# Kernel optimization log

Hardware: AMD Instinct MI355X
Metric: run time of the kernel (lower is better)

Reference implementation:

```python
import jax, jax.numpy as jnp
import numpy as np

F_SIZE = 8          # filter_size (even, >4 -> sinc mode)
C, H, W = 3, 720, 1280


def setup_inputs() -> dict:
    key = jax.random.key(0)
    k1, k2 = jax.random.split(key)
    x = jax.random.normal(k1, (1, C, H, W), dtype=jnp.float32)
    # optical flow in absolute pixels; a few pixels of motion is realistic
    flow = jax.random.normal(k2, (1, 2, H, W), dtype=jnp.float32) * 4.0
    return {"x": x, "flow": flow}


def _sinc_coeffs(s, offsets):
    # s: [H, W] fractional displacement in [0, 1); offsets: [F]
    # window * sinc interpolation coefficients -> [F, H, W]
    t = s[None, :, :] - offsets[:, None, None]
    return jnp.cos(jnp.pi * t / F_SIZE) * jnp.sinc(t)


def reference(x, flow):
    # Warper.forward in training mode (module default): q_flow = flow (no
    # fractional_accuracy rounding, which only applies in eval mode).
    _, C_, H_, W_ = x.shape
    fs = F_SIZE
    # neighbor tap offsets: -fs//2+1 .. fs//2  (e.g. -3..4 for fs=8)
    offsets = jnp.arange(-(fs // 2) + 1, fs // 2 + 1, dtype=jnp.float32)

    fx = flow[0, 0]  # horizontal (column) flow [H, W]
    fy = flow[0, 1]  # vertical (row) flow    [H, W]
    rfx = jnp.floor(fx)
    rfy = jnp.floor(fy)
    sx = fx - rfx    # fractional part in [0, 1)
    sy = fy - rfy

    col = jnp.arange(W_, dtype=jnp.float32)[None, :]   # [1, W]
    row = jnp.arange(H_, dtype=jnp.float32)[:, None]   # [H, 1]
    # integer neighbor coordinates, clamped (padding_mode='border') [F, H, W]
    ix = jnp.clip(col[None] + rfx[None] + offsets[:, None, None], 0, W_ - 1).astype(jnp.int32)
    iy = jnp.clip(row[None] + rfy[None] + offsets[:, None, None], 0, H_ - 1).astype(jnp.int32)

    x0 = x[0]  # [C, H, W]
    # multi-tap gather: [C, F_i, F_j, H, W] (nearest grid_sample of integer coords)
    gathered = x0[:, iy[:, None, :, :], ix[None, :, :, :]]

    cx = _sinc_coeffs(sx, offsets)  # [F, H, W] horizontal coefficients
    cy = _sinc_coeffs(sy, offsets)  # [F, H, W] vertical coefficients
    # separable interpolation: sum over j (columns) then i (rows), fused
    out = jnp.einsum('cijhw,jhw,ihw->chw', gathered, cx, cy)
    return out[None]  # [1, C, H, W]
```

## Files before the change

### kernel.cpp

```cpp
#include <hip/hip_runtime.h>
#include <math.h>

#define CC 3
#define HH 720
#define WW 1280
#define HW (HH * WW)

#define TW 64
#define TH 16
#define GX (WW / TW)
#define GY (HH / TH)
#define NWG (GX * GY)

#define SW 1288
#define PLANE (HH * SW)
#define WS_HALFS (6 * PLANE + 8)
#define WS_BYTES ((size_t)WS_HALFS * 2)

#define RMAX 16
#define NKEY 97

typedef float f4 __attribute__((ext_vector_type(4), aligned(4)));
typedef _Float16 h8 __attribute__((ext_vector_type(8), aligned(4)));
typedef _Float16 h2v __attribute__((ext_vector_type(2)));

#if __has_builtin(__builtin_amdgcn_fdot2)
#define HAVE_FDOT2 1
#endif

__constant__ float COSK[8] = {0.38268343f, 0.70710678f, 0.92387953f, 1.0f,
                              0.92387953f, 0.70710678f, 0.38268343f, 0.0f};
__constant__ float SINK[8] = {-0.92387953f, -0.70710678f, -0.38268343f, 0.0f,
                              0.38268343f, 0.70710678f, 0.92387953f, 1.0f};
__constant__ float SGNK[8] = {-1.0f, 1.0f, -1.0f, 1.0f, -1.0f, 1.0f, -1.0f, 1.0f};

__device__ __forceinline__ void sinc_weights(float s, float* wgt) {
    const float PI = 3.14159265358979f;
    float sp = __sinf(PI * s);
    float s8, c8;
    __sincosf(PI * s * 0.125f, &s8, &c8);
#pragma unroll
    for (int j = 0; j < 8; ++j) {
        float t = s - (float)(j - 3);
        float win = c8 * COSK[j] + s8 * SINK[j];
        float r = (t == 0.0f) ? 1.0f : __fdividef(sp * SGNK[j], PI * t);
        wgt[j] = win * r;
    }
}

__device__ __forceinline__ float dot8f(h8 v, const h2v* cw) {
#ifdef HAVE_FDOT2
    h2v* p = (h2v*)&v;
    float a = __builtin_amdgcn_fdot2(p[0], cw[0], 0.0f, false);
    a = __builtin_amdgcn_fdot2(p[1], cw[1], a, false);
    a = __builtin_amdgcn_fdot2(p[2], cw[2], a, false);
    a = __builtin_amdgcn_fdot2(p[3], cw[3], a, false);
    return a;
#else
    float r = 0.f;
#pragma unroll
    for (int j = 0; j < 8; ++j)
        r = fmaf((float)v[j], (float)cw[j >> 1][j & 1], r);
    return r;
#endif
}

__global__ __launch_bounds__(256) void conv_kernel(const float* __restrict__ x,
                                                   _Float16* __restrict__ ws) {
    int tid = blockIdx.x * blockDim.x + threadIdx.x;
    if (tid >= CC * HH * (WW / 4)) return;
    int k4 = tid % (WW / 4);
    int rest = tid / (WW / 4);
    int k = k4 * 4;
    f4 v = *(const f4*)(x + rest * WW + k);
    int dst = rest * SW + k;
    _Float16 a = (_Float16)v.x, b = (_Float16)v.y,
             c = (_Float16)v.z, d = (_Float16)v.w;
    typedef _Float16 h4 __attribute__((ext_vector_type(4), aligned(8)));
    *(h4*)(ws + dst) = (h4){a, b, c, d};
    _Float16* wb = ws + 3 * PLANE + 1 + dst;
    wb[0] = a; wb[1] = b; wb[2] = c; wb[3] = d;
}

__device__ __forceinline__ void pixel_slow(const float* __restrict__ x,
                                           int bx, int by,
                                           const float* cxw, const float* cyw,
                                           float& r0, float& r1, float& r2) {
    int xcl[8];
#pragma unroll
    for (int j = 0; j < 8; ++j) xcl[j] = min(max(bx + (j - 3), 0), WW - 1);
    r0 = 0.f; r1 = 0.f; r2 = 0.f;
#pragma unroll
    for (int i = 0; i < 8; ++i) {
        int o = min(max(by + (i - 3), 0), HH - 1) * WW;
        float cyi = cyw[i];
        const float* p0 = x + o;
        const float* p1 = p0 + HW;
        const float* p2 = p1 + HW;
        float rs0 = 0.f, rs1 = 0.f, rs2 = 0.f;
#pragma unroll
        for (int j = 0; j < 8; ++j) {
            float cj = cxw[j];
            rs0 = fmaf(p0[xcl[j]], cj, rs0);
            rs1 = fmaf(p1[xcl[j]], cj, rs1);
            rs2 = fmaf(p2[xcl[j]], cj, rs2);
        }
        r0 = fmaf(cyi, rs0, r0);
        r1 = fmaf(cyi, rs1, r1);
        r2 = fmaf(cyi, rs2, r2);
    }
}

__global__ __launch_bounds__(1024) void warp_kernel(const float* __restrict__ x,
                                                    const float* __restrict__ flow,
                                                    const _Float16* __restrict__ hx,
                                                    float* __restrict__ out) {
    __shared__ float sfx[1024], sfy[1024];
    __shared__ unsigned short sid[1024];
    __shared__ int HIST[128], SC[128], CUR[128];

    int tid = threadIdx.x;

    int bid = blockIdx.x;
    const int q = NWG / 8, r = NWG % 8;
    int xcd = bid & 7;
    int swz = (xcd < r ? xcd * (q + 1) : r * (q + 1) + (xcd - r) * q) + (bid >> 3);
    int tx = swz % GX;
    int ty = swz / GX;
    int w0 = tx * TW;
    int h0 = ty * TH;

    if (tid < 128) HIST[tid] = 0;
    __syncthreads();

    int w = w0 + (tid & 63);
    int h = h0 + (tid >> 6);
    int idx = h * WW + w;
    float fx = flow[idx];
    float fy = flow[HW + idx];
    sfx[tid] = fx;
    sfy[tid] = fy;
    {
        float rfx = floorf(fx), rfy = floorf(fy);
        int ix = (int)rfx, iy = (int)rfy;
        int s = w + ix - 3;
        int by = h + iy;
        bool fast = (iy >= -RMAX) && (iy <= RMAX) && (s >= 0) && (s <= WW - 8);
        int key = fast ? ((by - (h0 - RMAX)) * 2 + (s & 1)) : (NKEY - 1);
        atomicAdd(&HIST[key], 1);
    }
    __syncthreads();

    if (tid < 128) SC[tid] = HIST[tid];
    __syncthreads();
    for (int d = 1; d < 128; d <<= 1) {
        int v = 0;
        if (tid < 128 && tid >= d) v = SC[tid - d];
        __syncthreads();
        if (tid < 128) SC[tid] += v;
        __syncthreads();
    }
    if (tid < 128) CUR[tid] = SC[tid] - HIST[tid];
    __syncthreads();

    {
        float rfx = floorf(fx), rfy = floorf(fy);
        int ix = (int)rfx, iy = (int)rfy;
        int s = w + ix - 3;
        int by = h + iy;
        bool fast = (iy >= -RMAX) && (iy <= RMAX) && (s >= 0) && (s <= WW - 8);
        int key = fast ? ((by - (h0 - RMAX)) * 2 + (s & 1)) : (NKEY - 1);
        int pos = atomicAdd(&CUR[key], 1);
        sid[pos] = (unsigned short)tid;
    }
    __syncthreads();

    int me = sid[tid];
    float mfx = sfx[me], mfy = sfy[me];
    int mw = w0 + (me & 63);
    int mh = h0 + (me >> 6);
    float rfx = floorf(mfx), rfy = floorf(mfy);
    float sx = mfx - rfx, sy = mfy - rfy;
    int ix = (int)rfx, iy = (int)rfy;
    int s = mw + ix - 3;
    int by = mh + iy;
    bool fast = (iy >= -RMAX) && (iy <= RMAX) && (s >= 0) && (s <= WW - 8);

    float cxw[8], cyw[8];
    sinc_weights(sx, cxw);
    sinc_weights(sy, cyw);

    float r0, r1, r2;
    if (fast) {
        h2v cwp[4];
#pragma unroll
        for (int j = 0; j < 4; ++j)
            cwp[j] = (h2v){(_Float16)cxw[2 * j], (_Float16)cxw[2 * j + 1]};
        const _Float16* hp = hx + ((s & 1) ? (3 * PLANE + 1) : 0) + s;
        int ro[8];
#pragma unroll
        for (int i = 0; i < 8; ++i)
            ro[i] = min(max(by + (i - 3), 0), HH - 1) * SW;
        r0 = r1 = r2 = 0.f;
#pragma unroll
        for (int i = 0; i < 8; ++i) {
            h8 v0 = *(const h8*)(hp + ro[i]);
            h8 v1 = *(const h8*)(hp + ro[i] + PLANE);
            h8 v2 = *(const h8*)(hp + ro[i] + 2 * PLANE);
            float cyi = cyw[i];
            r0 = fmaf(cyi, dot8f(v0, cwp), r0);
            r1 = fmaf(cyi, dot8f(v1, cwp), r1);
            r2 = fmaf(cyi, dot8f(v2, cwp), r2);
        }
    } else {
        pixel_slow(x, mw + ix, mh + iy, cxw, cyw, r0, r1, r2);
    }

    int oidx = mh * WW + mw;
    out[oidx] = r0;
    out[HW + oidx] = r1;
    out[2 * HW + oidx] = r2;
}

__global__ __launch_bounds__(256) void warp_kernel_f32(const float* __restrict__ x,
                                                       const float* __restrict__ flow,
                                                       float* __restrict__ out) {
    int idx = blockIdx.x * blockDim.x + threadIdx.x;
    if (idx >= HW) return;
    int w = idx % WW;
    int h = idx / WW;
    float fx = flow[idx], fy = flow[HW + idx];
    float rfx = floorf(fx), rfy = floorf(fy);
    int bx = w + (int)rfx, by = h + (int)rfy;
    float cxw[8], cyw[8];
    sinc_weights(fx - rfx, cxw);
    sinc_weights(fy - rfy, cyw);
    float r0, r1, r2;
    pixel_slow(x, bx, by, cxw, cyw, r0, r1, r2);
    out[idx] = r0;
    out[HW + idx] = r1;
    out[2 * HW + idx] = r2;
}

extern "C" void kernel_launch(void* const* d_in, const int* in_sizes, int n_in,
                              void* d_out, int out_size, void* d_ws, size_t ws_size,
                              hipStream_t stream) {
    const float* x = (const float*)d_in[0];
    const float* flow = (const float*)d_in[1];
    float* out = (float*)d_out;

    if (ws_size >= WS_BYTES) {
        _Float16* ws = (_Float16*)d_ws;
        int nconv = CC * HH * (WW / 4);
        conv_kernel<<<(nconv + 255) / 256, 256, 0, stream>>>(x, ws);
        warp_kernel<<<NWG, 1024, 0, stream>>>(x, flow, ws, out);
    } else {
        warp_kernel_f32<<<(HW + 255) / 256, 256, 0, stream>>>(x, flow, out);
    }
}
```

Baseline: 53.93 us.

## Shrink warp tiles, use wave-shuffle scan, and software-pipeline fp16 channel loads

Halves the tile height so each block has 512 threads, and sizes the histogram keys to match. The multi-barrier LDS prefix scan becomes a single-wave shuffle scan, and the XCD swizzle is simplified because NWG is now divisible by 8. In the fast path, all row loads for one channel are issued before the sinc weights are computed, and each channel's loads overlap the previous channel's dot products. This hides gather latency and cuts barrier overhead, at the cost of more live registers for the v/u buffers.

```diff
diff --git a/kernel.cpp b/kernel.cpp
--- a/kernel.cpp
+++ b/kernel.cpp
@@ -7,10 +7,11 @@
 #define HW (HH * WW)
 
 #define TW 64
-#define TH 16
+#define TH 8
 #define GX (WW / TW)
 #define GY (HH / TH)
 #define NWG (GX * GY)
+#define NTHR 512
 
 #define SW 1288
 #define PLANE (HH * SW)
@@ -18,7 +19,8 @@
 #define WS_BYTES ((size_t)WS_HALFS * 2)
 
 #define RMAX 16
-#define NKEY 97
+#define NBY (TH + 2 * RMAX)
+#define NKEY (NBY * 2 + 1)
 
 typedef float f4 __attribute__((ext_vector_type(4), aligned(4)));
 typedef _Float16 h8 __attribute__((ext_vector_type(8), aligned(4)));
@@ -111,27 +113,24 @@
     }
 }
 
-__global__ __launch_bounds__(1024) void warp_kernel(const float* __restrict__ x,
+__global__ __launch_bounds__(NTHR) void warp_kernel(const float* __restrict__ x,
                                                     const float* __restrict__ flow,
                                                     const _Float16* __restrict__ hx,
                                                     float* __restrict__ out) {
-    __shared__ float sfx[1024], sfy[1024];
-    __shared__ unsigned short sid[1024];
-    __shared__ int HIST[128], SC[128], CUR[128];
+    __shared__ float sfx[NTHR], sfy[NTHR];
+    __shared__ unsigned short sid[NTHR];
+    __shared__ int HIST[128], CUR[128];
 
     int tid = threadIdx.x;
 
     int bid = blockIdx.x;
-    const int q = NWG / 8, r = NWG % 8;
-    int xcd = bid & 7;
-    int swz = (xcd < r ? xcd * (q + 1) : r * (q + 1) + (xcd - r) * q) + (bid >> 3);
+    int swz = (bid & 7) * (NWG / 8) + (bid >> 3);
     int tx = swz % GX;
     int ty = swz / GX;
     int w0 = tx * TW;
     int h0 = ty * TH;
 
     if (tid < 128) HIST[tid] = 0;
-    __syncthreads();
 
     int w = w0 + (tid & 63);
     int h = h0 + (tid >> 6);
@@ -140,36 +139,34 @@
     float fy = flow[HW + idx];
     sfx[tid] = fx;
     sfy[tid] = fy;
+    __syncthreads();
+
+    int key;
     {
-        float rfx = floorf(fx), rfy = floorf(fy);
-        int ix = (int)rfx, iy = (int)rfy;
+        int ix = (int)floorf(fx), iy = (int)floorf(fy);
         int s = w + ix - 3;
         int by = h + iy;
         bool fast = (iy >= -RMAX) && (iy <= RMAX) && (s >= 0) && (s <= WW - 8);
-        int key = fast ? ((by - (h0 - RMAX)) * 2 + (s & 1)) : (NKEY - 1);
-        atomicAdd(&HIST[key], 1);
-    }
-    __syncthreads();
-
-    if (tid < 128) SC[tid] = HIST[tid];
-    __syncthreads();
-    for (int d = 1; d < 128; d <<= 1) {
-        int v = 0;
-        if (tid < 128 && tid >= d) v = SC[tid - d];
-        __syncthreads();
-        if (tid < 128) SC[tid] += v;
-        __syncthreads();
-    }
-    if (tid < 128) CUR[tid] = SC[tid] - HIST[tid];
+        key = fast ? ((by - (h0 - RMAX)) * 2 + (s & 1)) : (NKEY - 1);
+    }
+    atomicAdd(&HIST[key], 1);
+    __syncthreads();
+
+    if (tid < 64) {
+        int a = HIST[2 * tid], b = HIST[2 * tid + 1];
+        int sum = a + b;
+#pragma unroll
+        for (int d = 1; d < 64; d <<= 1) {
+            int vv = __shfl_up(sum, d, 64);
+            if (tid >= d) sum += vv;
+        }
+        int excl = sum - a - b;
+        CUR[2 * tid] = excl;
+        CUR[2 * tid + 1] = excl + a;
+    }
     __syncthreads();
 
     {
-        float rfx = floorf(fx), rfy = floorf(fy);
-        int ix = (int)rfx, iy = (int)rfy;
-        int s = w + ix - 3;
-        int by = h + iy;
-        bool fast = (iy >= -RMAX) && (iy <= RMAX) && (s >= 0) && (s <= WW - 8);
-        int key = fast ? ((by - (h0 - RMAX)) * 2 + (s & 1)) : (NKEY - 1);
         int pos = atomicAdd(&CUR[key], 1);
         sid[pos] = (unsigned short)tid;
     }
@@ -186,33 +183,44 @@
     int by = mh + iy;
     bool fast = (iy >= -RMAX) && (iy <= RMAX) && (s >= 0) && (s <= WW - 8);
 
-    float cxw[8], cyw[8];
-    sinc_weights(sx, cxw);
-    sinc_weights(sy, cyw);
-
     float r0, r1, r2;
     if (fast) {
+        int ro[8];
+#pragma unroll
+        for (int i = 0; i < 8; ++i)
+            ro[i] = min(max(by + (i - 3), 0), HH - 1) * SW;
+        const _Float16* hp = hx + ((s & 1) ? (3 * PLANE + 1) : 0) + s;
+
+        h8 v[8], u[8];
+#pragma unroll
+        for (int i = 0; i < 8; ++i) v[i] = *(const h8*)(hp + ro[i]);
+
+        float cxw[8], cyw[8];
+        sinc_weights(sx, cxw);
+        sinc_weights(sy, cyw);
         h2v cwp[4];
 #pragma unroll
         for (int j = 0; j < 4; ++j)
             cwp[j] = (h2v){(_Float16)cxw[2 * j], (_Float16)cxw[2 * j + 1]};
-        const _Float16* hp = hx + ((s & 1) ? (3 * PLANE + 1) : 0) + s;
-        int ro[8];
+
+        r0 = r1 = r2 = 0.f;
+#pragma unroll
+        for (int i = 0; i < 8; ++i) {
+            u[i] = *(const h8*)(hp + ro[i] + PLANE);
+            r0 = fmaf(cyw[i], dot8f(v[i], cwp), r0);
+        }
+#pragma unroll
+        for (int i = 0; i < 8; ++i) {
+            v[i] = *(const h8*)(hp + ro[i] + 2 * PLANE);
+            r1 = fmaf(cyw[i], dot8f(u[i], cwp), r1);
+        }
 #pragma unroll
         for (int i = 0; i < 8; ++i)
-            ro[i] = min(max(by + (i - 3), 0), HH - 1) * SW;
-        r0 = r1 = r2 = 0.f;
-#pragma unroll
-        for (int i = 0; i < 8; ++i) {
-            h8 v0 = *(const h8*)(hp + ro[i]);
-            h8 v1 = *(const h8*)(hp + ro[i] + PLANE);
-            h8 v2 = *(const h8*)(hp + ro[i] + 2 * PLANE);
-            float cyi = cyw[i];
-            r0 = fmaf(cyi, dot8f(v0, cwp), r0);
-            r1 = fmaf(cyi, dot8f(v1, cwp), r1);
-            r2 = fmaf(cyi, dot8f(v2, cwp), r2);
-        }
+            r2 = fmaf(cyw[i], dot8f(v[i], cwp), r2);
     } else {
+        float cxw[8], cyw[8];
+        sinc_weights(sx, cxw);
+        sinc_weights(sy, cyw);
         pixel_slow(x, mw + ix, mh + iy, cxw, cyw, r0, r1, r2);
     }
 
@@ -253,7 +261,7 @@
         _Float16* ws = (_Float16*)d_ws;
         int nconv = CC * HH * (WW / 4);
         conv_kernel<<<(nconv + 255) / 256, 256, 0, stream>>>(x, ws);
-        warp_kernel<<<NWG, 1024, 0, stream>>>(x, flow, ws, out);
+        warp_kernel<<<NWG, NTHR, 0, stream>>>(x, flow, ws, out);
     } else {
         warp_kernel_f32<<<(HW + 255) / 256, 256, 0, stream>>>(x, flow, out);
     }
```

Result: faster. 50.54 us (-6.3%).
